# Performance work log

Measured on AMD Instinct MI355X. Metric: run time of the kernel, lower is better.

The kernel has to match this reference:

```python
import math
import jax, jax.numpy as jnp
import numpy as np

SR = 22050
FRAME_SIZE = 1025
MAX_FILTER_SIZE = 20
B, T = 16, 2048


def _build_transform_matrix(frame_size=FRAME_SIZE, sr=SR, max_filter_size=MAX_FILTER_SIZE):
    max_freq = sr / 2
    freq = np.linspace(0, max_freq, num=frame_size, endpoint=True)
    mel = 2595 * np.log10(1 + freq / 700)
    min_mel, max_mel = mel[0], mel[-1]
    raw = (mel - min_mel) / (max_mel - min_mel) * (max_filter_size - 1) + 1
    mtx = np.zeros((frame_size, frame_size), dtype=np.float32)
    for i in range(frame_size):
        fs = math.floor(raw[i]) // 2 * 2 + 1
        start, end = i - fs // 2, i + fs // 2 + 1
        start, end = max(0, start), min(end, frame_size)
        mtx[i, start:end] = 1.0 / (end - start)
    return jnp.asarray(mtx)


def setup_inputs() -> dict:
    key = jax.random.key(0)
    k1, k2 = jax.random.split(key)
    model_output = jax.random.normal(k1, (B, FRAME_SIZE, T), dtype=jnp.float32)
    target = jax.random.normal(k2, (B, FRAME_SIZE, T), dtype=jnp.float32)
    transform_matrix = _build_transform_matrix()
    return {"model_output": model_output, "target": target, "transform_matrix": transform_matrix}


def reference(model_output, target, transform_matrix):
    # db_to_amp(x)**2 == (10**(x/20))**2 == 10**(x/10)
    mo = jnp.power(10.0, model_output / 10.0)
    tg = jnp.power(10.0, target / 10.0)
    diff = mo - tg  # [B, F, T]
    # mel-scale variable-width mean filter applied as dense matmul, per original
    filtered = jnp.einsum('ij,bjt->bit', transform_matrix, diff)
    return jnp.mean(filtered ** 2)
```

## Files before the change

kernel.cpp:

```cpp
#include <hip/hip_runtime.h>


#define F 1025
#define TT 2048
#define BB 16
#define NSEG 12
#define SEG 86
#define RING 24
#define TPB 128
#define TCH 512
#define NTB (TT / TCH)
#define NBLK (BB * NTB * NSEG)
#define CHUNK 4
#define HALF 10

__global__ __launch_bounds__(TPB, 2) void mel_mse_kernel(const float* __restrict__ mo,
                                                         const float* __restrict__ tg,
                                                         const float* __restrict__ mtx,
                                                         double* __restrict__ partial) {
    const int tid = threadIdx.x;
    const int blk = blockIdx.x;
    const int s  = blk % NSEG;
    const int r_ = blk / NSEG;
    const int tb = r_ % NTB;
    const int b  = r_ / NTB;

    const int i0 = s * SEG;
    const int i1 = (i0 + SEG < F) ? (i0 + SEG) : F;
    const int nrows = i1 - i0;

    __shared__ float4 ring[RING * TPB];
    __shared__ int    be_l[SEG];
    __shared__ int    bs_l[SEG];
    __shared__ float  binv_l[SEG];

    for (int k = tid; k < nrows; k += TPB) {
        const int i  = i0 + k;
        const int c0 = (i - HALF > 0) ? (i - HALF) : 0;
        const int c1 = (i + HALF + 1 < F) ? (i + HALF + 1) : F;
        const float* mrow = mtx + (size_t)i * F;
        int first = -1, last = -1;
        float fv = 0.0f;
        for (int c = c0; c < c1; ++c) {
            const float v = mrow[c];
            if (v != 0.0f) {
                if (first < 0) { first = c; fv = v; }
                last = c;
            }
        }
        bs_l[k]   = first;
        be_l[k]   = last + 1;
        binv_l[k] = fv;
    }
    __syncthreads();

    const int jstart = bs_l[0];
    const int jend   = be_l[nrows - 1];

    const int ct = tb * TPB + tid;
    const float4* __restrict__ moP = (const float4*)(mo + (size_t)b * F * TT) + ct;
    const float4* __restrict__ tgP = (const float4*)(tg + (size_t)b * F * TT) + ct;
    const size_t rs = TT / 4;

    const float C = 0.33219281f;

    float4 A0[CHUNK], G0[CHUNK], A1[CHUNK], G1[CHUNK], A2[CHUNK], G2[CHUNK];

#define LOADC(Ad, Gd, jbase)                                        \
    _Pragma("unroll")                                               \
    for (int r = 0; r < CHUNK; ++r) {                               \
        int jr = (jbase) + r;                                       \
        jr = (jr < jend) ? jr : (jend - 1);                         \
        Ad[r] = moP[(size_t)jr * rs];                               \
        Gd[r] = tgP[(size_t)jr * rs];                               \
    }

    LOADC(A0, G0, jstart)
    LOADC(A1, G1, jstart + CHUNK)

    float wx = 0.0f, wy = 0.0f, wz = 0.0f, ww = 0.0f, acc = 0.0f;
    int i = 0, cs = jstart, wp = 0, rp = 0;

    for (int j = jstart; j < jend; j += CHUNK) {
        LOADC(A2, G2, j + 2 * CHUNK)
        #pragma unroll
        for (int r = 0; r < CHUNK; ++r) {
            if (j + r < jend) {
                const float dx = __builtin_amdgcn_exp2f(A0[r].x * C)
                               - __builtin_amdgcn_exp2f(G0[r].x * C);
                const float dy = __builtin_amdgcn_exp2f(A0[r].y * C)
                               - __builtin_amdgcn_exp2f(G0[r].y * C);
                const float dz = __builtin_amdgcn_exp2f(A0[r].z * C)
                               - __builtin_amdgcn_exp2f(G0[r].z * C);
                const float dw = __builtin_amdgcn_exp2f(A0[r].w * C)
                               - __builtin_amdgcn_exp2f(G0[r].w * C);
                float4 dv; dv.x = dx; dv.y = dy; dv.z = dz; dv.w = dw;
                ring[wp + tid] = dv;
                wp += TPB; if (wp == RING * TPB) wp = 0;
                wx += dx; wy += dy; wz += dz; ww += dw;
                while (i < nrows && be_l[i] <= j + r + 1) {
                    const int si = bs_l[i];
                    while (cs < si) {
                        const float4 o = ring[rp + tid];
                        rp += TPB; if (rp == RING * TPB) rp = 0;
                        wx -= o.x; wy -= o.y; wz -= o.z; ww -= o.w;
                        ++cs;
                    }
                    const float inv = binv_l[i];
                    const float fx = wx * inv, fy = wy * inv;
                    const float fz = wz * inv, fw = ww * inv;
                    acc = fmaf(fx, fx, fmaf(fy, fy, fmaf(fz, fz, fmaf(fw, fw, acc))));
                    ++i;
                }
            }
        }
        #pragma unroll
        for (int r = 0; r < CHUNK; ++r) {
            A0[r] = A1[r]; G0[r] = G1[r];
            A1[r] = A2[r]; G1[r] = G2[r];
        }
    }
#undef LOADC

    #pragma unroll
    for (int off = 32; off > 0; off >>= 1)
        acc += __shfl_down(acc, off, 64);

    __shared__ double wred[2];
    const int wid = tid >> 6, lane = tid & 63;
    if (lane == 0) wred[wid] = (double)acc;
    __syncthreads();
    if (tid == 0)
        partial[blk] = wred[0] + wred[1];
}

__global__ __launch_bounds__(256) void final_kernel(const double* __restrict__ partial,
                                                    float* __restrict__ out) {
    const int tid = threadIdx.x;
    double s = 0.0;
    for (int k = tid; k < NBLK; k += 256) s += partial[k];
    #pragma unroll
    for (int off = 32; off > 0; off >>= 1)
        s += __shfl_down(s, off, 64);
    __shared__ double wred[4];
    const int wid = tid >> 6, lane = tid & 63;
    if (lane == 0) wred[wid] = s;
    __syncthreads();
    if (tid == 0) {
        double tot = wred[0] + wred[1] + wred[2] + wred[3];
        out[0] = (float)(tot / ((double)BB * (double)F * (double)TT));
    }
}

extern "C" void kernel_launch(void* const* d_in, const int* in_sizes, int n_in,
                              void* d_out, int out_size, void* d_ws, size_t ws_size,
                              hipStream_t stream) {
    const float* mo  = (const float*)d_in[0];
    const float* tg  = (const float*)d_in[1];
    const float* mtx = (const float*)d_in[2];

    double* partial = (double*)d_ws;

    mel_mse_kernel<<<NBLK, TPB, 0, stream>>>(mo, tg, mtx, partial);
    final_kernel<<<1, 256, 0, stream>>>(partial, (float*)d_out);
}
```

Measured before the change: 63.52 us.

## Fuse final reduction via last-block atomic counter and prefetch before band setup

Replaces the separate final reduction kernel with a last-block-done pattern: each block publishes its partial atomically, increments a counter, and the last block sums all partials and writes the output. The input prefetch now starts before the per-row band computation from the matrix, using a statically known row window (i0-HALF to i1+HALF) instead of the data-dependent start and end, so global loads overlap the setup. This removes one kernel launch but adds a memset on the stream, and it may process a few extra rows outside the actual band range.

Result: slower. 77.37 us (+21.8%).

```diff
diff --git a/kernel.cpp b/kernel.cpp
--- a/kernel.cpp
+++ b/kernel.cpp
@@ -17,7 +17,9 @@
 __global__ __launch_bounds__(TPB, 2) void mel_mse_kernel(const float* __restrict__ mo,
                                                          const float* __restrict__ tg,
                                                          const float* __restrict__ mtx,
-                                                         double* __restrict__ partial) {
+                                                         double* __restrict__ partial,
+                                                         unsigned int* __restrict__ counter,
+                                                         float* __restrict__ out) {
     const int tid = threadIdx.x;
     const int blk = blockIdx.x;
     const int s  = blk % NSEG;
@@ -29,13 +31,35 @@
     const int i1 = (i0 + SEG < F) ? (i0 + SEG) : F;
     const int nrows = i1 - i0;
 
+    const int jA = (i0 - HALF > 0) ? (i0 - HALF) : 0;
+    const int jE = (i1 + HALF < F) ? (i1 + HALF) : F;
+
     __shared__ float4 ring[RING * TPB];
     __shared__ int    be_l[SEG];
     __shared__ int    bs_l[SEG];
     __shared__ float  binv_l[SEG];
 
-    for (int k = tid; k < nrows; k += TPB) {
-        const int i  = i0 + k;
+    const int ct = tb * TPB + tid;
+    const float4* __restrict__ moP = (const float4*)(mo + (size_t)b * F * TT) + ct;
+    const float4* __restrict__ tgP = (const float4*)(tg + (size_t)b * F * TT) + ct;
+    const size_t rs = TT / 4;
+
+    float4 A0[CHUNK], G0[CHUNK], A1[CHUNK], G1[CHUNK], A2[CHUNK], G2[CHUNK];
+
+#define LOADC(Ad, Gd, jbase)                                        \
+    _Pragma("unroll")                                               \
+    for (int r = 0; r < CHUNK; ++r) {                               \
+        int jr = (jbase) + r;                                       \
+        jr = (jr < jE) ? jr : (jE - 1);                             \
+        Ad[r] = moP[(size_t)jr * rs];                               \
+        Gd[r] = tgP[(size_t)jr * rs];                               \
+    }
+
+    LOADC(A0, G0, jA)
+    LOADC(A1, G1, jA + CHUNK)
+
+    if (tid < nrows) {
+        const int i  = i0 + tid;
         const int c0 = (i - HALF > 0) ? (i - HALF) : 0;
         const int c1 = (i + HALF + 1 < F) ? (i + HALF + 1) : F;
         const float* mrow = mtx + (size_t)i * F;
@@ -48,44 +72,22 @@
                 last = c;
             }
         }
-        bs_l[k]   = first;
-        be_l[k]   = last + 1;
-        binv_l[k] = fv;
+        bs_l[tid]   = first;
+        be_l[tid]   = last + 1;
+        binv_l[tid] = fv;
     }
     __syncthreads();
 
-    const int jstart = bs_l[0];
-    const int jend   = be_l[nrows - 1];
-
-    const int ct = tb * TPB + tid;
-    const float4* __restrict__ moP = (const float4*)(mo + (size_t)b * F * TT) + ct;
-    const float4* __restrict__ tgP = (const float4*)(tg + (size_t)b * F * TT) + ct;
-    const size_t rs = TT / 4;
-
     const float C = 0.33219281f;
 
-    float4 A0[CHUNK], G0[CHUNK], A1[CHUNK], G1[CHUNK], A2[CHUNK], G2[CHUNK];
+    float wx = 0.0f, wy = 0.0f, wz = 0.0f, ww = 0.0f, acc = 0.0f;
+    int i = 0, cs = jA, wp = 0, rp = 0;
 
-#define LOADC(Ad, Gd, jbase)                                        \
-    _Pragma("unroll")                                               \
-    for (int r = 0; r < CHUNK; ++r) {                               \
-        int jr = (jbase) + r;                                       \
-        jr = (jr < jend) ? jr : (jend - 1);                         \
-        Ad[r] = moP[(size_t)jr * rs];                               \
-        Gd[r] = tgP[(size_t)jr * rs];                               \
-    }
-
-    LOADC(A0, G0, jstart)
-    LOADC(A1, G1, jstart + CHUNK)
-
-    float wx = 0.0f, wy = 0.0f, wz = 0.0f, ww = 0.0f, acc = 0.0f;
-    int i = 0, cs = jstart, wp = 0, rp = 0;
-
-    for (int j = jstart; j < jend; j += CHUNK) {
+    for (int j = jA; j < jE; j += CHUNK) {
         LOADC(A2, G2, j + 2 * CHUNK)
         #pragma unroll
         for (int r = 0; r < CHUNK; ++r) {
-            if (j + r < jend) {
+            if (j + r < jE) {
                 const float dx = __builtin_amdgcn_exp2f(A0[r].x * C)
                                - __builtin_amdgcn_exp2f(G0[r].x * C);
                 const float dy = __builtin_amdgcn_exp2f(A0[r].y * C)
@@ -127,28 +129,36 @@
         acc += __shfl_down(acc, off, 64);
 
     __shared__ double wred[2];
+    __shared__ int s_done;
     const int wid = tid >> 6, lane = tid & 63;
     if (lane == 0) wred[wid] = (double)acc;
     __syncthreads();
-    if (tid == 0)
-        partial[blk] = wred[0] + wred[1];
-}
+    if (tid == 0) {
+        const double ps = wred[0] + wred[1];
+        atomicExch((unsigned long long*)&partial[blk], __double_as_longlong(ps));
+        __threadfence();
+        const unsigned int prev = atomicAdd(counter, 1u);
+        s_done = (prev == (unsigned int)(NBLK - 1));
+    }
+    __syncthreads();
 
-__global__ __launch_bounds__(256) void final_kernel(const double* __restrict__ partial,
-                                                    float* __restrict__ out) {
-    const int tid = threadIdx.x;
-    double s = 0.0;
-    for (int k = tid; k < NBLK; k += 256) s += partial[k];
-    #pragma unroll
-    for (int off = 32; off > 0; off >>= 1)
-        s += __shfl_down(s, off, 64);
-    __shared__ double wred[4];
-    const int wid = tid >> 6, lane = tid & 63;
-    if (lane == 0) wred[wid] = s;
-    __syncthreads();
-    if (tid == 0) {
-        double tot = wred[0] + wred[1] + wred[2] + wred[3];
-        out[0] = (float)(tot / ((double)BB * (double)F * (double)TT));
+    if (s_done) {
+        double sum = 0.0;
+        for (int k = tid; k < NBLK; k += TPB) {
+            const unsigned long long bits =
+                atomicAdd((unsigned long long*)&partial[k], 0ULL);
+            sum += __longlong_as_double(bits);
+        }
+        #pragma unroll
+        for (int off = 32; off > 0; off >>= 1)
+            sum += __shfl_down(sum, off, 64);
+        __shared__ double w2[2];
+        if (lane == 0) w2[wid] = sum;
+        __syncthreads();
+        if (tid == 0) {
+            const double tot = w2[0] + w2[1];
+            out[0] = (float)(tot / ((double)BB * (double)F * (double)TT));
+        }
     }
 }
 
@@ -159,8 +169,11 @@
     const float* tg  = (const float*)d_in[1];
     const float* mtx = (const float*)d_in[2];
 
-    double* partial = (double*)d_ws;
+    char* ws = (char*)d_ws;
+    double*       partial = (double*)ws;
+    unsigned int* counter = (unsigned int*)(ws + 8192);
 
-    mel_mse_kernel<<<NBLK, TPB, 0, stream>>>(mo, tg, mtx, partial);
-    final_kernel<<<1, 256, 0, stream>>>(partial, (float*)d_out);
+    hipMemsetAsync(counter, 0, sizeof(unsigned int), stream);
+    mel_mse_kernel<<<NBLK, TPB, 0, stream>>>(mo, tg, mtx, partial, counter,
+                                             (float*)d_out);
 }
```
